# Kernel tuning notes

Hardware: AMD Instinct MI355X
Metric: run time of the kernel (lower is better)

The kernel has to match this reference:

```python
import jax, jax.numpy as jnp
import numpy as np

B, T, C = 4, 2048, 1024


def setup_inputs() -> dict:
    key = jax.random.key(0)
    ks = jax.random.split(key, 5)
    s = 1.0 / np.sqrt(C)
    return {
        "X": jax.random.normal(ks[0], (B, T, C), dtype=jnp.float32),
        "Wq": jax.random.normal(ks[1], (C, C), dtype=jnp.float32) * s,
        "Wk": jax.random.normal(ks[2], (C, C), dtype=jnp.float32) * s,
        "Wv": jax.random.normal(ks[3], (C, C), dtype=jnp.float32) * s,
        "Wo": jax.random.normal(ks[4], (C, C), dtype=jnp.float32) * s,
    }


def reference(X, Wq, Wk, Wv, Wo):
    Bx, Tx, Cx = X.shape
    Q = X @ Wq  # [B,T,C]
    K = X @ Wk
    V = X @ Wv
    scores = jnp.einsum('btc,bsc->bts', Q, K) / jnp.sqrt(jnp.asarray(Cx, X.dtype))
    # causal mask: position t attends to s <= t
    causal = jnp.tril(jnp.ones((Tx, Tx), dtype=bool))
    scores = jnp.where(causal, scores, jnp.asarray(-jnp.inf, scores.dtype))
    weights = jax.nn.softmax(scores, axis=-1)
    out = jnp.einsum('bts,bsc->btc', weights, V)
    return out @ Wo
```

## Files before the change

kernel.cpp:

```cpp
#include <hip/hip_runtime.h>
#include <hip/hip_bf16.h>
#include <cmath>


typedef __attribute__((ext_vector_type(8))) __bf16 bf16x8;
typedef __attribute__((ext_vector_type(8))) short short8;
typedef __attribute__((ext_vector_type(4))) float f32x4;

__device__ __forceinline__ unsigned short f2bf(float f) {
  union { float f; unsigned u; } v; v.f = f;
  unsigned u = v.u;
  u += ((u >> 16) & 1u) + 0x7fffu;
  return (unsigned short)(u >> 16);
}
__device__ __forceinline__ float bf2f(unsigned short h) {
  union { unsigned u; float f; } v; v.u = ((unsigned)h) << 16;
  return v.f;
}

#define GLDS(gp, sp)                                                           \
  __builtin_amdgcn_global_load_lds(                                            \
      (const __attribute__((address_space(1))) void*)(gp),                     \
      (__attribute__((address_space(3))) void*)(sp), 16, 0, 0)

__global__ void prep(const float* __restrict__ X,
                     const float* __restrict__ w0, const float* __restrict__ w1,
                     const float* __restrict__ w2, const float* __restrict__ w3,
                     unsigned short* __restrict__ Xb,
                     unsigned short* __restrict__ wcat,
                     unsigned short* __restrict__ wot,
                     int n) {
  if (blockIdx.z < 4) {
    const float* src = blockIdx.z == 0 ? w0 : blockIdx.z == 1 ? w1
                       : blockIdx.z == 2 ? w2 : w3;
    unsigned short* dst =
        blockIdx.z < 3 ? wcat + (size_t)blockIdx.z * n * n : wot;
    __shared__ float tile[32][33];
    int bx = blockIdx.x * 32, by = blockIdx.y * 32;
    int tx = threadIdx.x, ty = threadIdx.y;
#pragma unroll
    for (int i = 0; i < 32; i += 8)
      tile[ty + i][tx] = src[(size_t)(by + ty + i) * n + bx + tx];
    __syncthreads();
#pragma unroll
    for (int i = 0; i < 32; i += 8)
      dst[(size_t)(bx + ty + i) * n + by + tx] = f2bf(tile[tx][ty + i]);
  } else {
    const int bid = (blockIdx.z - 4) * 1024 + blockIdx.y * 32 + blockIdx.x;
    const int t = threadIdx.y * 32 + threadIdx.x;
    const int i = (bid * 256 + t) * 4;
    float4 f = *(const float4*)(X + i);
    ushort4 o = make_ushort4(f2bf(f.x), f2bf(f.y), f2bf(f.z), f2bf(f.w));
    *(ushort4*)(Xb + i) = o;
  }
}

template <typename OutT, int NW>
__global__ __launch_bounds__(NW * 64, NW / 2)
void gemm_bt(const unsigned short* __restrict__ A, int lda, long long sA,
             const unsigned short* __restrict__ B, int ldb, long long sB,
             OutT* __restrict__ Cp, int ldc, long long sC,
             int K, float alpha, int tri, int kcap, int gx, int qkv) {
  A  += (long long)blockIdx.z * sA;
  B  += (long long)blockIdx.z * sB;
  Cp += (long long)blockIdx.z * sC;

  int by, bx;
  if (tri) {
    const int idx = blockIdx.x;
    by = (int)((sqrtf(8.f * idx + 1.f) - 1.f) * 0.5f);
    while (by * (by + 1) / 2 > idx) --by;
    while ((by + 1) * (by + 2) / 2 <= idx) ++by;
    bx = idx - by * (by + 1) / 2;
  } else if (gx > 0) {
    const int id = blockIdx.x;
    const int gs = gx * 8;
    const int g = id / gs, r = id - g * gs;
    bx = r >> 3;
    by = g * 8 + (r & 7);
    if (kcap) by = (gridDim.x / gx) - 1 - by;
  } else {
    by = blockIdx.y;
    bx = blockIdx.x;
  }
  const int m0 = by * 128;
  const int n0 = bx * 128;
  const int Keff = kcap ? min(K, m0 + 128) : K;

  const int tid  = threadIdx.x;
  const int lane = tid & 63;
  const int w    = tid >> 6;
  const int wm   = (NW == 4) ? (w >> 1) * 64 : (w >> 1) * 32;
  const int wn   = (w & 1) * 64;
  const int quad = lane >> 4;
  const int l16  = lane & 15;
  constexpr int AI = (NW == 4) ? 4 : 2;
  constexpr int NR = 128 / (NW * 8);

  __shared__ unsigned short As[8192];
  __shared__ unsigned short Bs[8192];

  f32x4 acc[AI][4];
#pragma unroll
  for (int i = 0; i < AI; ++i)
#pragma unroll
    for (int j = 0; j < 4; ++j)
      acc[i][j] = (f32x4){0.f, 0.f, 0.f, 0.f};

  const int srow = tid >> 3;
  const int scol = ((tid & 7) ^ (srow & 7)) * 8;
  const unsigned short* gA = A + (long long)(m0 + srow) * lda + scol;
  const unsigned short* gB = B + (long long)(n0 + srow) * ldb + scol;
  const int rsw = l16 & 7;

  for (int kt = 0; kt < Keff; kt += 64) {
    __syncthreads();
#pragma unroll
    for (int r = 0; r < NR; ++r) {
      GLDS(gA + (long long)(r * NW * 8) * lda + kt, As + r * NW * 512 + tid * 8);
      GLDS(gB + (long long)(r * NW * 8) * ldb + kt, Bs + r * NW * 512 + tid * 8);
    }
    __syncthreads();
#pragma unroll
    for (int ks = 0; ks < 2; ++ks) {
      bf16x8 af[AI], bfr[4];
#pragma unroll
      for (int i = 0; i < AI; ++i)
        af[i] = *(const bf16x8*)(As + (wm + i * 16 + l16) * 64 +
                                 ((ks * 4 + quad) ^ rsw) * 8);
#pragma unroll
      for (int j = 0; j < 4; ++j)
        bfr[j] = *(const bf16x8*)(Bs + (wn + j * 16 + l16) * 64 +
                                  ((ks * 4 + quad) ^ rsw) * 8);
#pragma unroll
      for (int i = 0; i < AI; ++i)
#pragma unroll
        for (int j = 0; j < 4; ++j)
          acc[i][j] = __builtin_amdgcn_mfma_f32_16x16x32_bf16(af[i], bfr[j],
                                                              acc[i][j], 0, 0, 0);
    }
  }

#pragma unroll
  for (int i = 0; i < AI; ++i) {
#pragma unroll
    for (int j = 0; j < 4; ++j) {
      const int row = m0 + wm + i * 16 + quad * 4;
      const int col = n0 + wn + j * 16 + l16;
      if constexpr (sizeof(OutT) == 2) {
        if (qkv) {
          if (col >= 2048) {
            const int b = row >> 11, t = row & 2047, cv = col - 2048;
            ushort4 o = make_ushort4(f2bf(acc[i][j][0]), f2bf(acc[i][j][1]),
                                     f2bf(acc[i][j][2]), f2bf(acc[i][j][3]));
            *(ushort4*)((unsigned short*)Cp + 16777216LL +
                        ((long long)(b * 1024 + cv)) * 2048 + t) = o;
          } else {
            unsigned short* dst =
                (unsigned short*)Cp + (col >= 1024 ? 8388608LL - 1024 : 0);
#pragma unroll
            for (int r = 0; r < 4; ++r)
              dst[(long long)(row + r) * 1024 + col] = f2bf(acc[i][j][r]);
          }
          continue;
        }
#pragma unroll
        for (int r = 0; r < 4; ++r)
          Cp[(long long)(row + r) * ldc + col] = (OutT)f2bf(acc[i][j][r] * alpha);
      } else {
#pragma unroll
        for (int r = 0; r < 4; ++r)
          Cp[(long long)(row + r) * ldc + col] = acc[i][j][r] * alpha;
      }
    }
  }
}

__global__ __launch_bounds__(256)
void softmax_causal(unsigned short* __restrict__ S, int T) {
  const long long row = blockIdx.x;
  const int t = (int)(row & (long long)(T - 1));
  const int limit = ((t >> 7) + 1) << 7;
  unsigned short* p = S + row * T;
  const int tid  = threadIdx.x;
  const int base = tid * 8;
  const bool active = base < limit;

  short8 raw = {};
  if (active) raw = *(const short8*)(p + base);
  float x[8];
  float mx = -1e30f;
#pragma unroll
  for (int j = 0; j < 8; ++j) {
    bool valid = active && (base + j) <= t;
    x[j] = valid ? bf2f((unsigned short)raw[j]) : -1e30f;
    mx = fmaxf(mx, x[j]);
  }
#pragma unroll
  for (int off = 32; off > 0; off >>= 1) mx = fmaxf(mx, __shfl_xor(mx, off));
  __shared__ float red[8];
  const int wv = tid >> 6;
  if ((tid & 63) == 0) red[wv] = mx;
  __syncthreads();
  mx = fmaxf(fmaxf(red[0], red[1]), fmaxf(red[2], red[3]));

  float sum = 0.f;
#pragma unroll
  for (int j = 0; j < 8; ++j) {
    bool valid = active && (base + j) <= t;
    x[j] = valid ? __expf(x[j] - mx) : 0.f;
    sum += x[j];
  }
#pragma unroll
  for (int off = 32; off > 0; off >>= 1) sum += __shfl_xor(sum, off);
  if ((tid & 63) == 0) red[4 + wv] = sum;
  __syncthreads();
  sum = red[4] + red[5] + red[6] + red[7];
  const float inv = 1.f / sum;

  if (active) {
    unsigned short out[8];
#pragma unroll
    for (int j = 0; j < 8; ++j) out[j] = f2bf(x[j] * inv);
    *(short8*)(p + base) = *(const short8*)out;
  }
}

extern "C" void kernel_launch(void* const* d_in, const int* in_sizes, int n_in,
                              void* d_out, int out_size, void* d_ws,
                              size_t ws_size, hipStream_t stream) {
  (void)in_sizes; (void)n_in; (void)out_size; (void)ws_size;
  const int Bb = 4, T = 2048, C = 1024;
  const int M = Bb * T;

  const float* X  = (const float*)d_in[0];
  const float* Wq = (const float*)d_in[1];
  const float* Wk = (const float*)d_in[2];
  const float* Wv = (const float*)d_in[3];
  const float* Wo = (const float*)d_in[4];
  float* Out = (float*)d_out;

  char* w = (char*)d_ws;
  unsigned short* Xb   = (unsigned short*)w; w += (size_t)M * C * 2;
  unsigned short* Wcat = (unsigned short*)w; w += (size_t)3 * C * C * 2;
  unsigned short* Wot  = (unsigned short*)w; w += (size_t)C * C * 2;
  unsigned short* Q    = (unsigned short*)w; w += (size_t)M * C * 2;
  unsigned short* Kb   = (unsigned short*)w; w += (size_t)M * C * 2;
  unsigned short* Vt   = (unsigned short*)w; w += (size_t)M * C * 2;
  unsigned short* O    = Xb;
  unsigned short* S    = (unsigned short*)d_out;

  prep<<<dim3(32, 32, 12), dim3(32, 8), 0, stream>>>(X, Wq, Wk, Wv, Wo, Xb,
                                                     Wcat, Wot, C);

  gemm_bt<unsigned short, 4><<<dim3((3 * C / 128) * (M / 128), 1, 1), dim3(256),
                               0, stream>>>(
      Xb, C, 0, Wcat, C, 0, Q, C, 0, C, 1.f, 0, 0, 3 * C / 128, 1);
  const int ntri = (T / 128) * (T / 128 + 1) / 2;
  gemm_bt<unsigned short, 8><<<dim3(ntri, 1, Bb), dim3(512), 0, stream>>>(
      Q, C, (long long)T * C, Kb, C, (long long)T * C,
      S, T, (long long)T * T, C, 0.03125f, 1, 0, 0, 0);
  softmax_causal<<<M, 256, 0, stream>>>(S, T);
  gemm_bt<unsigned short, 8><<<dim3((C / 128) * (T / 128), 1, Bb), dim3(512), 0,
                               stream>>>(
      S, T, (long long)T * T, Vt, T, (long long)C * T,
      O, C, (long long)T * C, T, 1.f, 0, 1, C / 128, 0);
  gemm_bt<float, 8><<<dim3((C / 128) * (M / 128), 1, 1), dim3(512), 0, stream>>>(
      O, C, 0, Wot, C, 0, Out, C, 0, C, 1.f, 0, 0, C / 128, 0);
}
```

Measured before the change: 270.3 us.

## Switch attention and output GEMMs to single-wave 64x64 tiles

Splits the QKV projection into its own dedicated kernel and replaces the 128x128, 8-wave GEMM used for QK^T, PV and the output projection with a single-wave 64x64 tile kernel. The causal masks now work at 64-row granularity, so less of the upper triangle is computed and more blocks exist to fill the GPU. The cost is much less reuse per block, more global and LDS traffic per FLOP, and 64-thread blocks that may underuse the CUs. The PV launch also drops the grouped blockIdx ordering and uses a plain 2D grid.

```diff
diff --git a/kernel.cpp b/kernel.cpp
--- a/kernel.cpp
+++ b/kernel.cpp
@@ -55,12 +55,97 @@
   }
 }
 
-template <typename OutT, int NW>
-__global__ __launch_bounds__(NW * 64, NW / 2)
-void gemm_bt(const unsigned short* __restrict__ A, int lda, long long sA,
-             const unsigned short* __restrict__ B, int ldb, long long sB,
-             OutT* __restrict__ Cp, int ldc, long long sC,
-             int K, float alpha, int tri, int kcap, int gx, int qkv) {
+__global__ __launch_bounds__(256, 2)
+void gemm_qkv(const unsigned short* __restrict__ A, int lda,
+              const unsigned short* __restrict__ B, int ldb,
+              unsigned short* __restrict__ Cp, int K, int gx) {
+  const int id = blockIdx.x;
+  const int gs = gx * 8;
+  const int g = id / gs, r = id - g * gs;
+  const int bx = r >> 3;
+  const int by = g * 8 + (r & 7);
+  const int m0 = by * 128;
+  const int n0 = bx * 128;
+
+  const int tid  = threadIdx.x;
+  const int lane = tid & 63;
+  const int w    = tid >> 6;
+  const int wm   = (w >> 1) * 64;
+  const int wn   = (w & 1) * 64;
+  const int quad = lane >> 4;
+  const int l16  = lane & 15;
+
+  __shared__ unsigned short As[8192];
+  __shared__ unsigned short Bs[8192];
+
+  f32x4 acc[4][4];
+#pragma unroll
+  for (int i = 0; i < 4; ++i)
+#pragma unroll
+    for (int j = 0; j < 4; ++j)
+      acc[i][j] = (f32x4){0.f, 0.f, 0.f, 0.f};
+
+  const int srow = tid >> 3;
+  const int scol = ((tid & 7) ^ (srow & 7)) * 8;
+  const unsigned short* gA = A + (long long)(m0 + srow) * lda + scol;
+  const unsigned short* gB = B + (long long)(n0 + srow) * ldb + scol;
+  const int rsw = l16 & 7;
+
+  for (int kt = 0; kt < K; kt += 64) {
+    __syncthreads();
+#pragma unroll
+    for (int r2 = 0; r2 < 4; ++r2) {
+      GLDS(gA + (long long)(r2 * 32) * lda + kt, As + r2 * 2048 + tid * 8);
+      GLDS(gB + (long long)(r2 * 32) * ldb + kt, Bs + r2 * 2048 + tid * 8);
+    }
+    __syncthreads();
+#pragma unroll
+    for (int ks = 0; ks < 2; ++ks) {
+      bf16x8 af[4], bfr[4];
+#pragma unroll
+      for (int i = 0; i < 4; ++i)
+        af[i] = *(const bf16x8*)(As + (wm + i * 16 + l16) * 64 +
+                                 ((ks * 4 + quad) ^ rsw) * 8);
+#pragma unroll
+      for (int j = 0; j < 4; ++j)
+        bfr[j] = *(const bf16x8*)(Bs + (wn + j * 16 + l16) * 64 +
+                                  ((ks * 4 + quad) ^ rsw) * 8);
+#pragma unroll
+      for (int i = 0; i < 4; ++i)
+#pragma unroll
+        for (int j = 0; j < 4; ++j)
+          acc[i][j] = __builtin_amdgcn_mfma_f32_16x16x32_bf16(af[i], bfr[j],
+                                                              acc[i][j], 0, 0, 0);
+    }
+  }
+
+#pragma unroll
+  for (int i = 0; i < 4; ++i) {
+#pragma unroll
+    for (int j = 0; j < 4; ++j) {
+      const int row = m0 + wm + i * 16 + quad * 4;
+      const int col = n0 + wn + j * 16 + l16;
+      if (col >= 2048) {
+        const int b = row >> 11, t = row & 2047, cv = col - 2048;
+        ushort4 o = make_ushort4(f2bf(acc[i][j][0]), f2bf(acc[i][j][1]),
+                                 f2bf(acc[i][j][2]), f2bf(acc[i][j][3]));
+        *(ushort4*)(Cp + 16777216LL + ((long long)(b * 1024 + cv)) * 2048 + t) = o;
+      } else {
+        unsigned short* dst = Cp + (col >= 1024 ? 8388608LL - 1024 : 0);
+#pragma unroll
+        for (int r2 = 0; r2 < 4; ++r2)
+          dst[(long long)(row + r2) * 1024 + col] = f2bf(acc[i][j][r2]);
+      }
+    }
+  }
+}
+
+template <typename OutT>
+__global__ __launch_bounds__(64, 2)
+void gemm64(const unsigned short* __restrict__ A, int lda, long long sA,
+            const unsigned short* __restrict__ B, int ldb, long long sB,
+            OutT* __restrict__ Cp, int ldc, long long sC,
+            int K, float alpha, int tri, int kcap) {
   A  += (long long)blockIdx.z * sA;
   B  += (long long)blockIdx.z * sB;
   Cp += (long long)blockIdx.z * sC;
@@ -72,68 +157,56 @@
     while (by * (by + 1) / 2 > idx) --by;
     while ((by + 1) * (by + 2) / 2 <= idx) ++by;
     bx = idx - by * (by + 1) / 2;
-  } else if (gx > 0) {
-    const int id = blockIdx.x;
-    const int gs = gx * 8;
-    const int g = id / gs, r = id - g * gs;
-    bx = r >> 3;
-    by = g * 8 + (r & 7);
-    if (kcap) by = (gridDim.x / gx) - 1 - by;
   } else {
     by = blockIdx.y;
     bx = blockIdx.x;
-  }
-  const int m0 = by * 128;
-  const int n0 = bx * 128;
-  const int Keff = kcap ? min(K, m0 + 128) : K;
-
-  const int tid  = threadIdx.x;
-  const int lane = tid & 63;
-  const int w    = tid >> 6;
-  const int wm   = (NW == 4) ? (w >> 1) * 64 : (w >> 1) * 32;
-  const int wn   = (w & 1) * 64;
+    if (kcap) by = gridDim.y - 1 - by;
+  }
+  const int m0 = by * 64;
+  const int n0 = bx * 64;
+  const int Keff = kcap ? min(K, m0 + 64) : K;
+
+  const int lane = threadIdx.x;
   const int quad = lane >> 4;
   const int l16  = lane & 15;
-  constexpr int AI = (NW == 4) ? 4 : 2;
-  constexpr int NR = 128 / (NW * 8);
-
-  __shared__ unsigned short As[8192];
-  __shared__ unsigned short Bs[8192];
-
-  f32x4 acc[AI][4];
-#pragma unroll
-  for (int i = 0; i < AI; ++i)
+  const int rsw  = l16 & 7;
+
+  __shared__ unsigned short As[4096];
+  __shared__ unsigned short Bs[4096];
+
+  f32x4 acc[4][4];
+#pragma unroll
+  for (int i = 0; i < 4; ++i)
 #pragma unroll
     for (int j = 0; j < 4; ++j)
       acc[i][j] = (f32x4){0.f, 0.f, 0.f, 0.f};
 
-  const int srow = tid >> 3;
-  const int scol = ((tid & 7) ^ (srow & 7)) * 8;
+  const int srow = lane >> 3;
+  const int scol = ((lane & 7) ^ (srow & 7)) * 8;
   const unsigned short* gA = A + (long long)(m0 + srow) * lda + scol;
   const unsigned short* gB = B + (long long)(n0 + srow) * ldb + scol;
-  const int rsw = l16 & 7;
 
   for (int kt = 0; kt < Keff; kt += 64) {
     __syncthreads();
 #pragma unroll
-    for (int r = 0; r < NR; ++r) {
-      GLDS(gA + (long long)(r * NW * 8) * lda + kt, As + r * NW * 512 + tid * 8);
-      GLDS(gB + (long long)(r * NW * 8) * ldb + kt, Bs + r * NW * 512 + tid * 8);
+    for (int r = 0; r < 8; ++r) {
+      GLDS(gA + (long long)(r * 8) * lda + kt, As + r * 512 + lane * 8);
+      GLDS(gB + (long long)(r * 8) * ldb + kt, Bs + r * 512 + lane * 8);
     }
     __syncthreads();
 #pragma unroll
     for (int ks = 0; ks < 2; ++ks) {
-      bf16x8 af[AI], bfr[4];
-#pragma unroll
-      for (int i = 0; i < AI; ++i)
-        af[i] = *(const bf16x8*)(As + (wm + i * 16 + l16) * 64 +
+      bf16x8 af[4], bfr[4];
+#pragma unroll
+      for (int i = 0; i < 4; ++i)
+        af[i] = *(const bf16x8*)(As + (i * 16 + l16) * 64 +
                                  ((ks * 4 + quad) ^ rsw) * 8);
 #pragma unroll
       for (int j = 0; j < 4; ++j)
-        bfr[j] = *(const bf16x8*)(Bs + (wn + j * 16 + l16) * 64 +
+        bfr[j] = *(const bf16x8*)(Bs + (j * 16 + l16) * 64 +
                                   ((ks * 4 + quad) ^ rsw) * 8);
 #pragma unroll
-      for (int i = 0; i < AI; ++i)
+      for (int i = 0; i < 4; ++i)
 #pragma unroll
         for (int j = 0; j < 4; ++j)
           acc[i][j] = __builtin_amdgcn_mfma_f32_16x16x32_bf16(af[i], bfr[j],
@@ -142,35 +215,18 @@
   }
 
 #pragma unroll
-  for (int i = 0; i < AI; ++i) {
+  for (int i = 0; i < 4; ++i) {
 #pragma unroll
     for (int j = 0; j < 4; ++j) {
-      const int row = m0 + wm + i * 16 + quad * 4;
-      const int col = n0 + wn + j * 16 + l16;
-      if constexpr (sizeof(OutT) == 2) {
-        if (qkv) {
-          if (col >= 2048) {
-            const int b = row >> 11, t = row & 2047, cv = col - 2048;
-            ushort4 o = make_ushort4(f2bf(acc[i][j][0]), f2bf(acc[i][j][1]),
-                                     f2bf(acc[i][j][2]), f2bf(acc[i][j][3]));
-            *(ushort4*)((unsigned short*)Cp + 16777216LL +
-                        ((long long)(b * 1024 + cv)) * 2048 + t) = o;
-          } else {
-            unsigned short* dst =
-                (unsigned short*)Cp + (col >= 1024 ? 8388608LL - 1024 : 0);
-#pragma unroll
-            for (int r = 0; r < 4; ++r)
-              dst[(long long)(row + r) * 1024 + col] = f2bf(acc[i][j][r]);
-          }
-          continue;
-        }
-#pragma unroll
-        for (int r = 0; r < 4; ++r)
-          Cp[(long long)(row + r) * ldc + col] = (OutT)f2bf(acc[i][j][r] * alpha);
-      } else {
-#pragma unroll
-        for (int r = 0; r < 4; ++r)
-          Cp[(long long)(row + r) * ldc + col] = acc[i][j][r] * alpha;
+      const int row = m0 + i * 16 + quad * 4;
+      const int col = n0 + j * 16 + l16;
+#pragma unroll
+      for (int r = 0; r < 4; ++r) {
+        float v = acc[i][j][r] * alpha;
+        if constexpr (sizeof(OutT) == 2)
+          Cp[(long long)(row + r) * ldc + col] = (OutT)f2bf(v);
+        else
+          Cp[(long long)(row + r) * ldc + col] = v;
       }
     }
   }
@@ -180,7 +236,7 @@
 void softmax_causal(unsigned short* __restrict__ S, int T) {
   const long long row = blockIdx.x;
   const int t = (int)(row & (long long)(T - 1));
-  const int limit = ((t >> 7) + 1) << 7;
+  const int limit = ((t >> 6) + 1) << 6;
   unsigned short* p = S + row * T;
   const int tid  = threadIdx.x;
   const int base = tid * 8;
@@ -253,18 +309,20 @@
   prep<<<dim3(32, 32, 12), dim3(32, 8), 0, stream>>>(X, Wq, Wk, Wv, Wo, Xb,
                                                      Wcat, Wot, C);
 
-  gemm_bt<unsigned short, 4><<<dim3((3 * C / 128) * (M / 128), 1, 1), dim3(256),
-                               0, stream>>>(
-      Xb, C, 0, Wcat, C, 0, Q, C, 0, C, 1.f, 0, 0, 3 * C / 128, 1);
-  const int ntri = (T / 128) * (T / 128 + 1) / 2;
-  gemm_bt<unsigned short, 8><<<dim3(ntri, 1, Bb), dim3(512), 0, stream>>>(
+  gemm_qkv<<<dim3((3 * C / 128) * (M / 128)), dim3(256), 0, stream>>>(
+      Xb, C, Wcat, C, Q, C, 3 * C / 128);
+
+  const int ntri = (T / 64) * (T / 64 + 1) / 2;
+  gemm64<unsigned short><<<dim3(ntri, 1, Bb), dim3(64), 0, stream>>>(
       Q, C, (long long)T * C, Kb, C, (long long)T * C,
-      S, T, (long long)T * T, C, 0.03125f, 1, 0, 0, 0);
+      S, T, (long long)T * T, C, 0.03125f, 1, 0);
+
   softmax_causal<<<M, 256, 0, stream>>>(S, T);
-  gemm_bt<unsigned short, 8><<<dim3((C / 128) * (T / 128), 1, Bb), dim3(512), 0,
-                               stream>>>(
+
+  gemm64<unsigned short><<<dim3(C / 64, T / 64, Bb), dim3(64), 0, stream>>>(
       S, T, (long long)T * T, Vt, T, (long long)C * T,
-      O, C, (long long)T * C, T, 1.f, 0, 1, C / 128, 0);
-  gemm_bt<float, 8><<<dim3((C / 128) * (M / 128), 1, 1), dim3(512), 0, stream>>>(
-      O, C, 0, Wot, C, 0, Out, C, 0, C, 1.f, 0, 0, C / 128, 0);
-}
+      O, C, (long long)T * C, T, 1.f, 0, 1);
+
+  gemm64<float><<<dim3(C / 64, M / 64, 1), dim3(64), 0, stream>>>(
+      O, C, 0, Wot, C, 0, Out, C, 0, C, 1.f, 0, 0);
+}
```

Result: slower. 282.2 us (+4.4%).
